# Kernel optimization log

Hardware: AMD Instinct MI355X
Metric: run time of the kernel (lower is better)

Reference implementation:

```python
import jax, jax.numpy as jnp
import numpy as np

N, E, D, H, ED = 50000, 800000, 128, 4, 64
C = D // H  # per-head channels
EPS = 1e-5


def setup_inputs() -> dict:
    key = jax.random.key(0)
    ks = jax.random.split(key, 16)
    s = 0.05
    return {
        "x": jax.random.normal(ks[0], (N, D), jnp.float32),
        "edge_index": jax.random.randint(ks[1], (2, E), 0, N, jnp.int64 if jax.config.jax_enable_x64 else jnp.int32),
        "edge_attr": jax.random.normal(ks[2], (E, ED), jnp.float32),
        "Wq": jax.random.normal(ks[3], (D, H * C), jnp.float32) * s,
        "bq": jnp.zeros((H * C,), jnp.float32),
        "Wk": jax.random.normal(ks[4], (D, H * C), jnp.float32) * s,
        "bk": jnp.zeros((H * C,), jnp.float32),
        "Wv": jax.random.normal(ks[5], (D, H * C), jnp.float32) * s,
        "bv": jnp.zeros((H * C,), jnp.float32),
        "We": jax.random.normal(ks[6], (ED, H * C), jnp.float32) * s,  # lin_edge, bias=False
        "Wskip": jax.random.normal(ks[7], (D, H * C), jnp.float32) * s,
        "bskip": jnp.zeros((H * C,), jnp.float32),
        "Wbeta": jax.random.normal(ks[8], (3 * H * C, 1), jnp.float32) * s,  # lin_beta, bias=False
        "gamma": jnp.ones((D,), jnp.float32),
        "beta_ln": jnp.zeros((D,), jnp.float32),
    }


def _transformer_conv(x, src, dst, edge_attr, Wq, bq, Wk, bk, Wv, bv, We, Wskip, bskip, Wbeta):
    q = (x @ Wq + bq).reshape(N, H, C)
    k = (x @ Wk + bk).reshape(N, H, C)
    v = (x @ Wv + bv).reshape(N, H, C)
    e = (edge_attr @ We).reshape(E, H, C)
    k_j = k[src] + e                     # [E,H,C]
    v_j = v[src] + e                     # [E,H,C]
    alpha = jnp.einsum("ehc,ehc->eh", q[dst], k_j) / jnp.sqrt(jnp.float32(C))
    # per-destination softmax over incoming edges
    m = jax.ops.segment_max(alpha, dst, num_segments=N)          # [N,H]
    m = jnp.where(jnp.isfinite(m), m, 0.0)
    a = jnp.exp(alpha - m[dst])
    denom = jax.ops.segment_sum(a, dst, num_segments=N)          # [N,H]
    alpha = a / jnp.where(denom > 0, denom, 1.0)[dst]
    out = jax.ops.segment_sum(alpha[:, :, None] * v_j, dst, num_segments=N)  # [N,H,C]
    out = out.reshape(N, H * C)
    # beta-gated skip (beta=True, root_weight)
    x_r = x @ Wskip + bskip
    b = jax.nn.sigmoid(jnp.concatenate([out, x_r, out - x_r], axis=-1) @ Wbeta)  # [N,1]
    return b * x_r + (1.0 - b) * out


def reference(x, edge_index, edge_attr, Wq, bq, Wk, bk, Wv, bv, We, Wskip, bskip, Wbeta, gamma, beta_ln):
    src, dst = edge_index[0], edge_index[1]
    res = _transformer_conv(x, src, dst, edge_attr, Wq, bq, Wk, bk, Wv, bv, We, Wskip, bskip, Wbeta)
    out = jax.nn.gelu(res, approximate=False) + x
    mu = jnp.mean(out, axis=-1, keepdims=True)
    var = jnp.var(out, axis=-1, keepdims=True)
    return (out - mu) * jax.lax.rsqrt(var + EPS) * gamma + beta_ln
```

## Files before the change

kernel.cpp:

```cpp
#include <hip/hip_runtime.h>
#include <math.h>

#define NN 50000
#define EE 800000

typedef __bf16 bf16x8 __attribute__((ext_vector_type(8)));
typedef float f32x4 __attribute__((ext_vector_type(4)));
typedef float f32x2 __attribute__((ext_vector_type(2)));
typedef unsigned short ushort_t;
typedef unsigned int uint_t;

__device__ inline ushort_t f2bf(float f) {
  uint_t u = __float_as_uint(f);
  uint_t r = (u + 0x7fffu + ((u >> 16) & 1u)) >> 16;
  return (ushort_t)r;
}
__device__ inline float bflo(uint_t u) { return __uint_as_float(u << 16); }
__device__ inline float bfhi(uint_t u) { return __uint_as_float(u & 0xffff0000u); }

__device__ inline uint_t pk4_fp8(float a0, float a1, float a2, float a3) {
  a0 = fminf(fmaxf(a0, -448.f), 448.f);
  a1 = fminf(fmaxf(a1, -448.f), 448.f);
  a2 = fminf(fmaxf(a2, -448.f), 448.f);
  a3 = fminf(fmaxf(a3, -448.f), 448.f);
  uint_t lo = (uint_t)__builtin_amdgcn_cvt_pk_fp8_f32(a0, a1, 0, false) & 0xFFFFu;
  uint_t hi = (uint_t)__builtin_amdgcn_cvt_pk_fp8_f32(a2, a3, 0, false) & 0xFFFFu;
  return lo | (hi << 16);
}

__device__ inline void wave_sync() {
  asm volatile("s_waitcnt lgkmcnt(0)" ::: "memory");
  __builtin_amdgcn_wave_barrier();
}

__global__ __launch_bounds__(256) void k_prepA(const float* __restrict__ Wbeta,
                                               float* __restrict__ wcomb,
                                               int* __restrict__ counts) {
  int b = blockIdx.x;
  int o = threadIdx.x;
  if (b == 0) {
    if (o < 128) {
      wcomb[o]       = Wbeta[o]       + Wbeta[256 + o];
      wcomb[128 + o] = Wbeta[128 + o] - Wbeta[256 + o];
    }
  } else {
    int i = (b - 1) * 256 + o;
    if (i < NN) counts[i] = 0;
  }
}

__global__ __launch_bounds__(256) void k_prepB(
    const float* __restrict__ Wq, const float* __restrict__ Wk,
    const float* __restrict__ Wv, const float* __restrict__ Ws,
    const float* __restrict__ bq, const float* __restrict__ bk,
    const float* __restrict__ bv, const float* __restrict__ bs,
    ushort_t* __restrict__ Wbt, float* __restrict__ bcat,
    const float* __restrict__ We, ushort_t* __restrict__ WebT,
    const int* __restrict__ ei, int* __restrict__ counts) {
  int b = blockIdx.x;
  if (b >= 288) {
    int i = (b - 288) * 256 + threadIdx.x;
    if (i < EE) atomicAdd(&counts[ei[EE + i]], 1);
    return;
  }
  if (b >= 256) {
    int i = (b - 256) * 256 + threadIdx.x;
    int c = i >> 6, k = i & 63;
    WebT[c * 64 + k] = f2bf(We[k * 128 + c]);
    return;
  }
  int i = b * 256 + threadIdx.x;
  int c = i >> 7, k = i & 127;
  float w;
  if (c < 128)      w = Wq[k * 128 + c];
  else if (c < 256) w = Wk[k * 128 + (c - 128)];
  else if (c < 384) w = Wv[k * 128 + (c - 256)];
  else              w = Ws[k * 128 + (c - 384)];
  Wbt[(size_t)c * 128 + k] = f2bf(w);
  if (i < 512) {
    float bb;
    if (i < 128)      bb = bq[i];
    else if (i < 256) bb = bk[i - 128];
    else if (i < 384) bb = bv[i - 256];
    else              bb = bs[i - 384];
    bcat[i] = bb;
  }
}

__global__ __launch_bounds__(256) void k_mm(const float* __restrict__ x,
                                            const ushort_t* __restrict__ Wbt,
                                            const float* __restrict__ bcat,
                                            float* __restrict__ nqx,
                                            ushort_t* __restrict__ kb,
                                            ushort_t* __restrict__ vb) {
  __shared__ ushort_t As[128 * 128];
  __shared__ ushort_t Bs[128 * 128];
  int t = threadIdx.x;
  int rb = blockIdx.x * 128;
  int cb = blockIdx.y * 128;

  for (int q = t; q < 2048; q += 256) {
    int r = q >> 4, j = q & 15;
    int row = rb + r;
    float4 f0 = make_float4(0.f, 0.f, 0.f, 0.f), f1 = f0;
    if (row < NN) {
      const float4* xp = (const float4*)&x[(size_t)row * 128 + j * 8];
      f0 = xp[0]; f1 = xp[1];
    }
    uint_t u0 = (uint_t)f2bf(f0.x) | ((uint_t)f2bf(f0.y) << 16);
    uint_t u1 = (uint_t)f2bf(f0.z) | ((uint_t)f2bf(f0.w) << 16);
    uint_t u2 = (uint_t)f2bf(f1.x) | ((uint_t)f2bf(f1.y) << 16);
    uint_t u3 = (uint_t)f2bf(f1.z) | ((uint_t)f2bf(f1.w) << 16);
    int e = r * 128 + ((j * 8) ^ ((r & 7) << 3));
    *(uint4*)&As[e] = make_uint4(u0, u1, u2, u3);
  }
  for (int q = t; q < 2048; q += 256) {
    int c = q >> 4, j = q & 15;
    uint4 w = *(const uint4*)&Wbt[(size_t)(cb + c) * 128 + j * 8];
    int e = c * 128 + ((j * 8) ^ ((c & 7) << 3));
    *(uint4*)&Bs[e] = w;
  }
  __syncthreads();

  int lane = t & 63;
  int wv = t >> 6;
  int wr = wv >> 1, wc = wv & 1;
  int l15 = lane & 15, l4 = lane >> 4;

  f32x4 acc[4][4];
#pragma unroll
  for (int i = 0; i < 4; ++i)
#pragma unroll
    for (int j = 0; j < 4; ++j) acc[i][j] = (f32x4){0.f, 0.f, 0.f, 0.f};

#pragma unroll
  for (int ks = 0; ks < 4; ++ks) {
    int kbv = ks * 32 + l4 * 8;
    bf16x8 af[4], bfr[4];
#pragma unroll
    for (int i = 0; i < 4; ++i) {
      int r = wr * 64 + i * 16 + l15;
      af[i] = *(const bf16x8*)&As[r * 128 + (kbv ^ ((r & 7) << 3))];
    }
#pragma unroll
    for (int j = 0; j < 4; ++j) {
      int c = wc * 64 + j * 16 + l15;
      bfr[j] = *(const bf16x8*)&Bs[c * 128 + (kbv ^ ((c & 7) << 3))];
    }
#pragma unroll
    for (int i = 0; i < 4; ++i)
#pragma unroll
      for (int j = 0; j < 4; ++j)
        acc[i][j] = __builtin_amdgcn_mfma_f32_16x16x32_bf16(af[i], bfr[j], acc[i][j], 0, 0, 0);
  }

#pragma unroll
  for (int j = 0; j < 4; ++j) {
    int colg = cb + wc * 64 + j * 16 + l15;
    float bv = bcat[colg];
#pragma unroll
    for (int i = 0; i < 4; ++i) {
#pragma unroll
      for (int reg = 0; reg < 4; ++reg) {
        int grow = rb + wr * 64 + i * 16 + l4 * 4 + reg;
        if (grow < NN) {
          float val = acc[i][j][reg] + bv;
          if (cb == 0)        nqx[(size_t)grow * 256 + colg] = val;
          else if (cb == 128) kb[(size_t)grow * 128 + (colg - 128)] = f2bf(val);
          else if (cb == 256) vb[(size_t)grow * 128 + (colg - 256)] = f2bf(val);
          else                nqx[(size_t)grow * 256 + (colg - 256)] = val;
        }
      }
    }
  }
}

__global__ __launch_bounds__(1024) void k_scan(int* __restrict__ counts, int* __restrict__ offsets) {
  __shared__ int wsum[16];
  __shared__ int s_carry;
  int4* counts4 = (int4*)counts;
  int4* offsets4 = (int4*)offsets;
  int t = threadIdx.x, lane = t & 63, w = t >> 6;
  if (t == 0) s_carry = 0;
  __syncthreads();
  for (int base = 0; base < 12500; base += 1024) {
    int idx = base + t;
    int4 v = (idx < 12500) ? counts4[idx] : make_int4(0, 0, 0, 0);
    int e1 = v.x, e2 = e1 + v.y, e3 = e2 + v.z, tot = e3 + v.w;
    int s = tot;
#pragma unroll
    for (int off = 1; off < 64; off <<= 1) {
      int u = __shfl_up(s, off);
      if (lane >= off) s += u;
    }
    if (lane == 63) wsum[w] = s;
    __syncthreads();
    if (t == 0) {
      int ex = s_carry;
#pragma unroll
      for (int i = 0; i < 16; ++i) { int tv = wsum[i]; wsum[i] = ex; ex += tv; }
      s_carry = ex;
    }
    __syncthreads();
    int be = wsum[w] + s - tot;
    if (idx < 12500) {
      int4 o = make_int4(be, be + e1, be + e2, be + e3);
      offsets4[idx] = o;
      counts4[idx] = o;
    }
    __syncthreads();
  }
  if (t == 0) offsets[NN] = s_carry;
}

__global__ __launch_bounds__(256) void k_fillw(const int* __restrict__ ei,
                                               int* __restrict__ cursors,
                                               const float* __restrict__ ea,
                                               const ushort_t* __restrict__ WebT,
                                               int* __restrict__ srcs,
                                               unsigned char* __restrict__ eaWperm) {
  __shared__ ushort_t As[64 * 64];
  __shared__ ushort_t Bs[128 * 64];
  __shared__ float Ds[64][68];
  __shared__ int sP[64];
  int t = threadIdx.x;
  int eb = blockIdx.x * 64;

  if (t < 64) {
    int e = eb + t;
    int d = ei[EE + e];
    int p = atomicAdd(&cursors[d], 1);
    sP[t] = p;
    srcs[p] = ei[e];
  }
  for (int q = t; q < 512; q += 256) {
    int r = q >> 3, j = q & 7;
    const float4* xp = (const float4*)&ea[(size_t)(eb + r) * 64 + j * 8];
    float4 f0 = xp[0], f1 = xp[1];
    uint_t u0 = (uint_t)f2bf(f0.x) | ((uint_t)f2bf(f0.y) << 16);
    uint_t u1 = (uint_t)f2bf(f0.z) | ((uint_t)f2bf(f0.w) << 16);
    uint_t u2 = (uint_t)f2bf(f1.x) | ((uint_t)f2bf(f1.y) << 16);
    uint_t u3 = (uint_t)f2bf(f1.z) | ((uint_t)f2bf(f1.w) << 16);
    *(uint4*)&As[r * 64 + ((j * 8) ^ ((r & 7) << 3))] = make_uint4(u0, u1, u2, u3);
  }
  for (int q = t; q < 1024; q += 256) {
    int c = q >> 3, j = q & 7;
    uint4 w = *(const uint4*)&WebT[(size_t)c * 64 + j * 8];
    *(uint4*)&Bs[c * 64 + ((j * 8) ^ ((c & 7) << 3))] = w;
  }
  __syncthreads();

  int lane = t & 63, wv = t >> 6;
  int l15 = lane & 15, l4 = lane >> 4;
  f32x4 acc[4][2];
#pragma unroll
  for (int i = 0; i < 4; ++i)
#pragma unroll
    for (int j = 0; j < 2; ++j) acc[i][j] = (f32x4){0.f, 0.f, 0.f, 0.f};

#pragma unroll
  for (int ks = 0; ks < 2; ++ks) {
    int kbv = ks * 32 + l4 * 8;
    bf16x8 af[4], bfr[2];
#pragma unroll
    for (int i = 0; i < 4; ++i) {
      int r = i * 16 + l15;
      af[i] = *(const bf16x8*)&As[r * 64 + (kbv ^ ((r & 7) << 3))];
    }
#pragma unroll
    for (int j = 0; j < 2; ++j) {
      int c = wv * 32 + j * 16 + l15;
      bfr[j] = *(const bf16x8*)&Bs[c * 64 + (kbv ^ ((c & 7) << 3))];
    }
#pragma unroll
    for (int i = 0; i < 4; ++i)
#pragma unroll
      for (int j = 0; j < 2; ++j)
        acc[i][j] = __builtin_amdgcn_mfma_f32_16x16x32_bf16(af[i], bfr[j], acc[i][j], 0, 0, 0);
  }

#pragma unroll
  for (int half = 0; half < 2; ++half) {
    __syncthreads();
    if ((wv >> 1) == half) {
      int cbl = (wv & 1) * 32;
#pragma unroll
      for (int i = 0; i < 4; ++i)
#pragma unroll
        for (int j = 0; j < 2; ++j)
#pragma unroll
          for (int r = 0; r < 4; ++r)
            Ds[i * 16 + l4 * 4 + r][cbl + j * 16 + l15] = acc[i][j][r];
    }
    __syncthreads();
    int edge = t >> 2, seg = t & 3;
    const float* dr = &Ds[edge][seg * 16];
    uint_t wo[4];
#pragma unroll
    for (int i = 0; i < 4; ++i)
      wo[i] = pk4_fp8(dr[4 * i + 0], dr[4 * i + 1], dr[4 * i + 2], dr[4 * i + 3]);
    int p = sP[edge];
    *(uint4*)&eaWperm[(size_t)p * 128 + half * 64 + seg * 16] =
        make_uint4(wo[0], wo[1], wo[2], wo[3]);
  }
}

__global__ __launch_bounds__(256) void k_attn(
    const float* __restrict__ nqx,
    const ushort_t* __restrict__ kb, const ushort_t* __restrict__ vb,
    const unsigned char* __restrict__ eaWperm,
    const int* __restrict__ offsets, const int* __restrict__ srcs,
    const float* __restrict__ x, const float* __restrict__ wcomb,
    const float* __restrict__ gamma, const float* __restrict__ beta_ln,
    float* __restrict__ out) {
  __shared__ float sQ[4][128];
  __shared__ unsigned char sEA[4][16][144];
  __shared__ float sA[4][64];
  __shared__ int   sS[4][16];

  int t = threadIdx.x, wv = t >> 6, l = t & 63;
  int n = blockIdx.x * 4 + wv;
  int h = l >> 4, m = l & 15;
  int c0 = 2 * l, c1 = c0 + 1;
  const float scale = 0.17677669529663687f;

  const float* nrow = nqx + (size_t)n * 256;
  float2 q2 = *(const float2*)&nrow[c0];
  *(float2*)&sQ[wv][c0] = make_float2(q2.x * scale, q2.y * scale);
  if (l < 16) sS[wv][l] = 0;

  int js = offsets[n], je = offsets[n + 1];
  float acc0 = 0.f, acc1 = 0.f, lsum = 0.f;

  for (int base = js; base < je; base += 16) {
    int nj = je - base; if (nj > 16) nj = 16;
    wave_sync();

    uint4 e0 = {0,0,0,0}, e1 = {0,0,0,0};
    uint4 k0 = {0,0,0,0}, k1 = {0,0,0,0}, k2 = {0,0,0,0}, k3 = {0,0,0,0};
    if (m < nj) {
      int s = srcs[base + m];
      const uint4* erow = (const uint4*)(eaWperm + (size_t)(base + m) * 128 + 32 * h);
      e0 = erow[0]; e1 = erow[1];
      const uint4* krow = (const uint4*)(kb + (size_t)s * 128 + 32 * h);
      k0 = krow[0]; k1 = krow[1]; k2 = krow[2]; k3 = krow[3];
      if (h == 0) sS[wv][m] = s;
    }
    *(uint4*)&sEA[wv][m][32 * h]      = e0;
    *(uint4*)&sEA[wv][m][32 * h + 16] = e1;
    wave_sync();

    float z = 0.f;
    {
      const float* qp = &sQ[wv][32 * h];
      uint_t eu[8] = {e0.x, e0.y, e0.z, e0.w, e1.x, e1.y, e1.z, e1.w};
      uint_t ku[16] = {k0.x, k0.y, k0.z, k0.w, k1.x, k1.y, k1.z, k1.w,
                       k2.x, k2.y, k2.z, k2.w, k3.x, k3.y, k3.z, k3.w};
#pragma unroll
      for (int u = 0; u < 8; ++u) {
        f32x2 elo = __builtin_amdgcn_cvt_pk_f32_fp8(eu[u] & 0xFFFFu, false);
        f32x2 ehi = __builtin_amdgcn_cvt_pk_f32_fp8(eu[u] >> 16, false);
        float4 q4 = *(const float4*)&qp[4 * u];
        z += q4.x * (bflo(ku[2 * u]) + elo.x)
           + q4.y * (bfhi(ku[2 * u]) + elo.y)
           + q4.z * (bflo(ku[2 * u + 1]) + ehi.x)
           + q4.w * (bfhi(ku[2 * u + 1]) + ehi.y);
      }
    }
    float a = (m < nj) ? __expf(z) : 0.0f;
    lsum += a;
    sA[wv][l] = a;
    wave_sync();

    {
      int4 s0 = *(const int4*)&sS[wv][0];
      int4 s1 = *(const int4*)&sS[wv][4];
      f32x4 a0 = *(const f32x4*)&sA[wv][16 * h];
      f32x4 a1 = *(const f32x4*)&sA[wv][16 * h + 4];
      uint_t vv[8];
      int sidx[8] = {s0.x, s0.y, s0.z, s0.w, s1.x, s1.y, s1.z, s1.w};
#pragma unroll
      for (int e = 0; e < 8; ++e)
        vv[e] = *(const uint_t*)(vb + (size_t)sidx[e] * 128 + c0);
#pragma unroll
      for (int e = 0; e < 8; ++e) {
        float ae = (e < 4) ? a0[e] : a1[e - 4];
        uint_t ew = (uint_t)*(const ushort_t*)&sEA[wv][e][2 * l];
        f32x2 ef = __builtin_amdgcn_cvt_pk_f32_fp8(ew, false);
        acc0 += ae * (bflo(vv[e]) + ef.x);
        acc1 += ae * (bfhi(vv[e]) + ef.y);
      }
    }
    if (nj > 8) {
      int4 s2 = *(const int4*)&sS[wv][8];
      int4 s3 = *(const int4*)&sS[wv][12];
      f32x4 a2 = *(const f32x4*)&sA[wv][16 * h + 8];
      f32x4 a3 = *(const f32x4*)&sA[wv][16 * h + 12];
      uint_t vv[8];
      int sidx[8] = {s2.x, s2.y, s2.z, s2.w, s3.x, s3.y, s3.z, s3.w};
#pragma unroll
      for (int e = 0; e < 8; ++e)
        vv[e] = *(const uint_t*)(vb + (size_t)sidx[e] * 128 + c0);
#pragma unroll
      for (int e = 0; e < 8; ++e) {
        float ae = (e < 4) ? a2[e] : a3[e - 4];
        uint_t ew = (uint_t)*(const ushort_t*)&sEA[wv][8 + e][2 * l];
        f32x2 ef = __builtin_amdgcn_cvt_pk_f32_fp8(ew, false);
        acc0 += ae * (bflo(vv[e]) + ef.x);
        acc1 += ae * (bfhi(vv[e]) + ef.y);
      }
    }
  }

  lsum += __shfl_xor(lsum, 1); lsum += __shfl_xor(lsum, 2);
  lsum += __shfl_xor(lsum, 4); lsum += __shfl_xor(lsum, 8);

  float inv = (lsum > 0.f) ? (1.0f / lsum) : 1.0f;
  float o0 = acc0 * inv;
  float o1 = acc1 * inv;

  float2 xrv = *(const float2*)&nrow[128 + c0];
  float bp = o0 * wcomb[c0] + o1 * wcomb[c1] + xrv.x * wcomb[128 + c0] + xrv.y * wcomb[128 + c1];
#pragma unroll
  for (int off = 32; off > 0; off >>= 1) bp += __shfl_xor(bp, off);
  float bgate = 1.0f / (1.0f + __expf(-bp));
  float r0 = bgate * xrv.x + (1.0f - bgate) * o0;
  float r1 = bgate * xrv.y + (1.0f - bgate) * o1;

  float2 xv = *(const float2*)&x[(size_t)n * 128 + c0];
  float ge0 = 0.5f * r0 * (1.0f + erff(r0 * 0.70710678118654752f)) + xv.x;
  float ge1 = 0.5f * r1 * (1.0f + erff(r1 * 0.70710678118654752f)) + xv.y;

  float s1 = ge0 + ge1;
  float s2 = ge0 * ge0 + ge1 * ge1;
#pragma unroll
  for (int off = 32; off > 0; off >>= 1) {
    s1 += __shfl_xor(s1, off);
    s2 += __shfl_xor(s2, off);
  }
  float mean = s1 * (1.0f / 128.0f);
  float var = s2 * (1.0f / 128.0f) - mean * mean;
  float rstd = rsqrtf(var + 1e-5f);
  float2 ov;
  ov.x = (ge0 - mean) * rstd * gamma[c0] + beta_ln[c0];
  ov.y = (ge1 - mean) * rstd * gamma[c1] + beta_ln[c1];
  *(float2*)&out[(size_t)n * 128 + c0] = ov;
}

extern "C" void kernel_launch(void* const* d_in, const int* in_sizes, int n_in,
                              void* d_out, int out_size, void* d_ws, size_t ws_size,
                              hipStream_t stream) {
  const float* x   = (const float*)d_in[0];
  const int*   ei  = (const int*)d_in[1];
  const float* ea  = (const float*)d_in[2];
  const float* Wq  = (const float*)d_in[3];
  const float* bq  = (const float*)d_in[4];
  const float* Wk  = (const float*)d_in[5];
  const float* bk  = (const float*)d_in[6];
  const float* Wv  = (const float*)d_in[7];
  const float* bv  = (const float*)d_in[8];
  const float* We  = (const float*)d_in[9];
  const float* Wsk = (const float*)d_in[10];
  const float* bsk = (const float*)d_in[11];
  const float* Wb  = (const float*)d_in[12];
  const float* gamma = (const float*)d_in[13];
  const float* beta  = (const float*)d_in[14];
  float* out = (float*)d_out;

  char* cur = (char*)d_ws;
  auto alloc = [&](size_t bytes) {
    void* p = (void*)cur;
    cur += (bytes + 255) & ~(size_t)255;
    return p;
  };
  float*         nqx     = (float*)alloc((size_t)NN * 256 * 4);
  ushort_t*      kbuf    = (ushort_t*)alloc((size_t)NN * 128 * 2);
  ushort_t*      vbuf    = (ushort_t*)alloc((size_t)NN * 128 * 2);
  unsigned char* eaWperm = (unsigned char*)alloc((size_t)EE * 128);
  int*           srcs    = (int*)alloc((size_t)EE * 4);
  float*         wcomb   = (float*)alloc(256 * 4);
  float*         bcat    = (float*)alloc(512 * 4);
  ushort_t*      Wbt     = (ushort_t*)alloc((size_t)512 * 128 * 2);
  ushort_t*      WebT    = (ushort_t*)alloc((size_t)128 * 64 * 2);
  int*           counts  = (int*)alloc((size_t)NN * 4);
  int*           offsets = (int*)alloc((size_t)(NN + 4) * 4);

  k_prepA<<<197, 256, 0, stream>>>(Wb, wcomb, counts);
  k_prepB<<<288 + 3125, 256, 0, stream>>>(Wq, Wk, Wv, Wsk, bq, bk, bv, bsk,
                                          Wbt, bcat, We, WebT, ei, counts);
  k_mm<<<dim3(391, 4), 256, 0, stream>>>(x, Wbt, bcat, nqx, kbuf, vbuf);
  k_scan<<<1, 1024, 0, stream>>>(counts, offsets);
  k_fillw<<<12500, 256, 0, stream>>>(ei, counts, ea, WebT, srcs, eaWperm);
  k_attn<<<12500, 256, 0, stream>>>(nqx, kbuf, vbuf, eaWperm, offsets, srcs,
                                    x, wcomb, gamma, beta, out);
}
```

Before: 333.5 us.

## Restructure edge-feature MFMA so each wave owns 16 edges, packing FP8 in registers

The edge-attribute projection in the fill kernel is rearranged so each wave computes all 128 output channels for its own 16 edges, using the transposed MFMA product with weights as the A operand. Accumulators are packed to FP8 directly in registers and staged through the reused As buffer with wave-level syncs only. This removes the 17KB float Ds staging buffer and the block-wide barriers, lowering LDS use and synchronisation. The risk is that wave_sync must give correct intra-wave LDS ordering, and that overwriting As is safe only because each wave touches only its own rows.

```diff
diff --git a/kernel.cpp b/kernel.cpp
--- a/kernel.cpp
+++ b/kernel.cpp
@@ -221,7 +221,6 @@
                                                unsigned char* __restrict__ eaWperm) {
   __shared__ ushort_t As[64 * 64];
   __shared__ ushort_t Bs[128 * 64];
-  __shared__ float Ds[64][68];
   __shared__ int sP[64];
   int t = threadIdx.x;
   int eb = blockIdx.x * 64;
@@ -252,57 +251,44 @@
 
   int lane = t & 63, wv = t >> 6;
   int l15 = lane & 15, l4 = lane >> 4;
-  f32x4 acc[4][2];
-#pragma unroll
-  for (int i = 0; i < 4; ++i)
-#pragma unroll
-    for (int j = 0; j < 2; ++j) acc[i][j] = (f32x4){0.f, 0.f, 0.f, 0.f};
-
+  int edge = wv * 16 + l15;
+
+  bf16x8 bfr[2];
 #pragma unroll
   for (int ks = 0; ks < 2; ++ks) {
     int kbv = ks * 32 + l4 * 8;
-    bf16x8 af[4], bfr[2];
-#pragma unroll
-    for (int i = 0; i < 4; ++i) {
-      int r = i * 16 + l15;
-      af[i] = *(const bf16x8*)&As[r * 64 + (kbv ^ ((r & 7) << 3))];
-    }
-#pragma unroll
-    for (int j = 0; j < 2; ++j) {
-      int c = wv * 32 + j * 16 + l15;
-      bfr[j] = *(const bf16x8*)&Bs[c * 64 + (kbv ^ ((c & 7) << 3))];
-    }
-#pragma unroll
-    for (int i = 0; i < 4; ++i)
-#pragma unroll
-      for (int j = 0; j < 2; ++j)
-        acc[i][j] = __builtin_amdgcn_mfma_f32_16x16x32_bf16(af[i], bfr[j], acc[i][j], 0, 0, 0);
-  }
-
-#pragma unroll
-  for (int half = 0; half < 2; ++half) {
-    __syncthreads();
-    if ((wv >> 1) == half) {
-      int cbl = (wv & 1) * 32;
-#pragma unroll
-      for (int i = 0; i < 4; ++i)
-#pragma unroll
-        for (int j = 0; j < 2; ++j)
-#pragma unroll
-          for (int r = 0; r < 4; ++r)
-            Ds[i * 16 + l4 * 4 + r][cbl + j * 16 + l15] = acc[i][j][r];
-    }
-    __syncthreads();
-    int edge = t >> 2, seg = t & 3;
-    const float* dr = &Ds[edge][seg * 16];
-    uint_t wo[4];
-#pragma unroll
-    for (int i = 0; i < 4; ++i)
-      wo[i] = pk4_fp8(dr[4 * i + 0], dr[4 * i + 1], dr[4 * i + 2], dr[4 * i + 3]);
-    int p = sP[edge];
-    *(uint4*)&eaWperm[(size_t)p * 128 + half * 64 + seg * 16] =
-        make_uint4(wo[0], wo[1], wo[2], wo[3]);
-  }
+    bfr[ks] = *(const bf16x8*)&As[edge * 64 + (kbv ^ ((edge & 7) << 3))];
+  }
+
+  f32x4 acc[8];
+#pragma unroll
+  for (int i = 0; i < 8; ++i) acc[i] = (f32x4){0.f, 0.f, 0.f, 0.f};
+
+#pragma unroll
+  for (int ks = 0; ks < 2; ++ks) {
+    int kbv = ks * 32 + l4 * 8;
+#pragma unroll
+    for (int i = 0; i < 8; ++i) {
+      int c = i * 16 + l15;
+      bf16x8 af = *(const bf16x8*)&Bs[c * 64 + (kbv ^ ((c & 7) << 3))];
+      acc[i] = __builtin_amdgcn_mfma_f32_16x16x32_bf16(af, bfr[ks], acc[i], 0, 0, 0);
+    }
+  }
+
+  wave_sync();
+  uint_t* dst32 = (uint_t*)As;
+#pragma unroll
+  for (int i = 0; i < 8; ++i)
+    dst32[edge * 32 + i * 4 + l4] = pk4_fp8(acc[i][0], acc[i][1], acc[i][2], acc[i][3]);
+  wave_sync();
+
+  int el = wv * 16 + (lane >> 2), seg = lane & 3;
+  const uint4* srow = (const uint4*)((const unsigned char*)As + el * 128 + seg * 16);
+  uint4 lo = srow[0];
+  uint4 hi = srow[4];
+  int p = sP[el];
+  *(uint4*)&eaWperm[(size_t)p * 128 + seg * 16]      = lo;
+  *(uint4*)&eaWperm[(size_t)p * 128 + seg * 16 + 64] = hi;
 }
 
 __global__ __launch_bounds__(256) void k_attn(
```

New measurement: 311.1 us. 1.07x faster.
